# Kernel tuning notes

Hardware: AMD Instinct MI355X
Metric: run time of the kernel (lower is better)

## Reference

```python
import jax, jax.numpy as jnp
import numpy as np

F_DIM = 256
DFF = 2048      # torch TransformerEncoderLayer default dim_feedforward
NHEAD = 4
NCLS = 7
MAXLEN = 256
BATCH = 256
LN_EPS = 1e-5


def _layer_norm(x, g, b):
    m = x.mean(-1, keepdims=True)
    v = ((x - m) ** 2).mean(-1, keepdims=True)
    return (x - m) / jnp.sqrt(v + LN_EPS) * g + b


def _pos_encoding(n, d):
    # NOTE: original code builds PE over x.size(1) (the batch dim) -- kept faithfully.
    pos = jnp.arange(n, dtype=jnp.float32)[:, None]
    div = jnp.exp(jnp.arange(0, d, 2, dtype=jnp.float32) * (-np.log(10000.0) / d))
    pe = jnp.zeros((n, d), dtype=jnp.float32)
    pe = pe.at[:, 0::2].set(jnp.sin(pos * div))
    pe = pe.at[:, 1::2].set(jnp.cos(pos * div))
    return pe


def _mha(x, Wqkv, bqkv, Wo, bo):
    # x: [S, B, F]  (torch MHA default seq-first layout)
    S, B, F = x.shape
    hd = F // NHEAD
    qkv = x @ Wqkv.T + bqkv                      # [S, B, 3F]
    q, k, v = jnp.split(qkv, 3, axis=-1)
    rs = lambda t: t.reshape(S, B, NHEAD, hd).transpose(1, 2, 0, 3)  # [B, h, S, hd]
    q, k, v = rs(q), rs(k), rs(v)
    attn = jax.nn.softmax(jnp.einsum('bhsd,bhtd->bhst', q, k) / jnp.float32(np.sqrt(hd)), axis=-1)
    o = jnp.einsum('bhst,bhtd->bhsd', attn, v).transpose(2, 0, 1, 3).reshape(S, B, F)
    return o @ Wo.T + bo


def _forward(U_s, U_p, W_emb, b_emb, Wqkv, bqkv, Wo, bo, ln1_g, ln1_b,
             W1, b1, W2, b2, ln2_g, ln2_b, W_fc, b_fc, W_sm, b_sm, seq_lengths):
    L = np.asarray(seq_lengths)                   # static host lengths
    T, B, F = U_s.shape
    mask = jnp.arange(T)[:, None] < jnp.asarray(L)[None, :]        # [T, B] valid-turn mask
    bank_s = U_s * mask[:, :, None]               # zero-padded, as feature_transfer does
    # ---- ReasonMod / MultiTurnTransformer (post-LN encoder layer, eval mode) ----
    h = bank_s @ W_emb.T + b_emb
    h = h + _pos_encoding(B, F)                   # faithful quirk: PE over batch dim
    a_out = _mha(h, Wqkv, bqkv, Wo, bo)
    h1 = _layer_norm(h + a_out, ln1_g, ln1_b)
    ff = jax.nn.relu(h1 @ W1.T + b1) @ W2.T + b2
    h2 = _layer_norm(h1 + ff, ln2_g, ln2_b)
    q = h + h2                                    # [T, B, F]; identical for every t in the loop
    # ---- gather + segment-softmax + scatter-add attention pooling, all t at once ----
    e = jnp.einsum('ibf,tbf->tib', U_p, q)        # scores per (target t, turn i, conv b)
    e = jnp.where(mask[None, :, :], e, -1e30)
    a = jax.nn.softmax(e, axis=1) * mask[None, :, :]
    r = jnp.einsum('tib,ibf->tbf', a, U_p * mask[:, :, None])      # scatter_add equivalent
    rc = jnp.concatenate([bank_s, r], axis=-1)    # [T, B, 2F]
    hidden = jax.nn.relu(rc @ W_fc.T + b_fc)
    logp = jax.nn.log_softmax(hidden @ W_sm.T + b_sm, axis=2)      # [T, B, n_classes]
    rows = np.concatenate([np.arange(l) for l in L])
    cols = np.repeat(np.arange(B), L)
    return logp[rows, cols]                       # [total_tokens, n_classes]


def setup_inputs() -> dict:
    key = jax.random.key(0)
    ks = jax.random.split(key, 24)
    rn = lambda k, shape, s=0.05: jax.random.normal(k, shape, dtype=jnp.float32) * s
    F, D2 = F_DIM, 2 * F_DIM
    inp = {
        'U_s': jax.random.normal(ks[0], (MAXLEN, BATCH, F), dtype=jnp.float32),
        'U_p': jax.random.normal(ks[1], (MAXLEN, BATCH, F), dtype=jnp.float32),
        'W_emb': rn(ks[2], (F, F)), 'b_emb': jnp.zeros((F,), jnp.float32),
        'Wqkv': rn(ks[3], (3 * F, F)), 'bqkv': jnp.zeros((3 * F,), jnp.float32),
        'Wo': rn(ks[4], (F, F)), 'bo': jnp.zeros((F,), jnp.float32),
        'ln1_g': jnp.ones((F,), jnp.float32), 'ln1_b': jnp.zeros((F,), jnp.float32),
        'W1': rn(ks[5], (DFF, F)), 'b1': jnp.zeros((DFF,), jnp.float32),
        'W2': rn(ks[6], (F, DFF)), 'b2': jnp.zeros((F,), jnp.float32),
        'ln2_g': jnp.ones((F,), jnp.float32), 'ln2_b': jnp.zeros((F,), jnp.float32),
        'W_fc': rn(ks[7], (D2, D2)), 'b_fc': jnp.zeros((D2,), jnp.float32),
        'W_sm': rn(ks[8], (NCLS, D2)), 'b_sm': jnp.zeros((NCLS,), jnp.float32),
        'seq_lengths': jax.random.randint(ks[9], (BATCH,), MAXLEN // 2, MAXLEN + 1),
    }
    return inp


def reference(U_s, U_p, W_emb, b_emb, Wqkv, bqkv, Wo, bo, ln1_g, ln1_b,
              W1, b1, W2, b2, ln2_g, ln2_b, W_fc, b_fc, W_sm, b_sm, seq_lengths):
    return _forward(U_s, U_p, W_emb, b_emb, Wqkv, bqkv, Wo, bo, ln1_g, ln1_b,
                    W1, b1, W2, b2, ln2_g, ln2_b, W_fc, b_fc, W_sm, b_sm, seq_lengths)
```

## Files before the change

### kernel.cpp

```cpp
#include <hip/hip_runtime.h>

#define MTB 65536

typedef unsigned int uint;
typedef unsigned short ushort;

typedef _Float16 h8 __attribute__((ext_vector_type(8)));
typedef __attribute__((ext_vector_type(4))) float f4;

enum { E_BIAS=1, E_RELU=2, E_ACC=4, E_RES=8, E_PE=16, E_MASKA=32 };

__device__ __forceinline__ float ldsc(const float* p) { return *p; }
__device__ __forceinline__ float ldsc(const _Float16* p) { return (float)*p; }

__device__ __forceinline__ h8 uint4_to_h8(uint4 u) { return __builtin_bit_cast(h8, u); }

template<int EPI, int AMODE, int BMODE, typename CT, int CPL, typename RT, int RPL, int SWZ>
__global__ __launch_bounds__(256) void gemm_h(
    int M, int N, int K,
    const void* __restrict__ Ap, const void* __restrict__ Ap2, int lda, long batchA,
    const void* __restrict__ Bp, int ldw, long batchW,
    CT* __restrict__ C, long cplane, int ldc, long batchC,
    const float* __restrict__ bias,
    const RT* __restrict__ res, const RT* __restrict__ resLo,
    const float* __restrict__ pe,
    const int* __restrict__ seqlen)
{
    __shared__ _Float16 Ah[128][40];
    __shared__ _Float16 Al[(AMODE==3)?128:1][40];
    __shared__ _Float16 Bh[128][40];
    __shared__ _Float16 Bl[(BMODE==0)?128:1][40];

    const int z = blockIdx.z;
    C += (size_t)z * batchC;
    const float*    Af  = (const float*)Ap + (AMODE==0 ? (size_t)z*batchA : 0);
    const _Float16* Ahp = (const _Float16*)Ap + ((AMODE==2||AMODE==3) ? (size_t)z*batchA : 0);
    const _Float16* Alp = (const _Float16*)Ap2 + (AMODE==3 ? (size_t)z*batchA : 0);
    const float*    Bf  = (const float*)Bp + (BMODE!=2 ? (size_t)z*batchW : 0);
    const _Float16* Bhp = (const _Float16*)Bp;

    int bx = blockIdx.x, by = blockIdx.y;
    if (SWZ) {
        const int gx = gridDim.x;
        const int nwg = gx * gridDim.y;
        const int per = nwg >> 3;
        const int id = by * gx + bx;
        const int nid = (id & 7) * per + (id >> 3);
        bx = nid % gx; by = nid / gx;
    }
    const int m0 = by * 128, n0 = bx * 128;
    const int tid = threadIdx.x;
    const int lane = tid & 63, wid = tid >> 6;
    const int wr = wid >> 1, wc = wid & 1;

    f4 acc[4][4];
    {
        f4 zr = {0.f, 0.f, 0.f, 0.f};
        #pragma unroll
        for (int i = 0; i < 4; i++)
            #pragma unroll
            for (int j = 0; j < 4; j++) acc[i][j] = zr;
    }

    for (int k0 = 0; k0 < K; k0 += 32) {
        __syncthreads();
        if (AMODE == 0 || (AMODE == 4 && k0 < 256)) {
            #pragma unroll
            for (int i = 0; i < 4; i++) {
                const int row = i*32 + (tid>>3);
                const int cg  = (tid&7)<<2;
                const int m = m0 + row;
                float4 v; v.x=0.f; v.y=0.f; v.z=0.f; v.w=0.f;
                bool ok = true;
                if (EPI & E_MASKA) ok = ((m>>8) < seqlen[m&255]);
                if (ok) v = *(const float4*)(Af + (size_t)m*lda + k0 + cg);
                Ah[row][cg+0] = (_Float16)v.x;
                Ah[row][cg+1] = (_Float16)v.y;
                Ah[row][cg+2] = (_Float16)v.z;
                Ah[row][cg+3] = (_Float16)v.w;
            }
        } else if (AMODE == 4) {
            const _Float16* Ar = (const _Float16*)Ap2;
            const int row = tid >> 1;
            const int cg  = (tid & 1) << 4;
            const size_t off = (size_t)(m0 + row) * 256 + (k0 - 256) + cg;
            *(uint4*)&Ah[row][cg]     = *(const uint4*)(Ar + off);
            *(uint4*)&Ah[row][cg + 8] = *(const uint4*)(Ar + off + 8);
        } else {
            const int row = tid >> 1;
            const int cg  = (tid & 1) << 4;
            const size_t off = (size_t)(m0 + row) * lda + k0 + cg;
            *(uint4*)&Ah[row][cg]     = *(const uint4*)(Ahp + off);
            *(uint4*)&Ah[row][cg + 8] = *(const uint4*)(Ahp + off + 8);
            if (AMODE == 3) {
                *(uint4*)&Al[row][cg]     = *(const uint4*)(Alp + off);
                *(uint4*)&Al[row][cg + 8] = *(const uint4*)(Alp + off + 8);
            }
        }
        if (BMODE == 2) {
            const int row = tid >> 1;
            const int cg  = (tid & 1) << 4;
            const size_t off = (size_t)(n0 + row) * ldw + k0 + cg;
            *(uint4*)&Bh[row][cg]     = *(const uint4*)(Bhp + off);
            *(uint4*)&Bh[row][cg + 8] = *(const uint4*)(Bhp + off + 8);
        } else if (BMODE == 0) {
            #pragma unroll
            for (int i = 0; i < 4; i++) {
                const int row = i*32 + (tid>>3);
                const int cg  = (tid&7)<<2;
                float4 v = *(const float4*)(Bf + (size_t)(n0+row)*ldw + k0 + cg);
                _Float16 h0 = (_Float16)v.x, h1 = (_Float16)v.y,
                         h2 = (_Float16)v.z, h3 = (_Float16)v.w;
                Bh[row][cg+0]=h0; Bl[row][cg+0]=(_Float16)(v.x-(float)h0);
                Bh[row][cg+1]=h1; Bl[row][cg+1]=(_Float16)(v.y-(float)h1);
                Bh[row][cg+2]=h2; Bl[row][cg+2]=(_Float16)(v.z-(float)h2);
                Bh[row][cg+3]=h3; Bl[row][cg+3]=(_Float16)(v.w-(float)h3);
            }
        } else if (BMODE == 3) {
            #pragma unroll
            for (int i = 0; i < 4; i++) {
                const int row = i*32 + (tid>>3);
                const int cg  = (tid&7)<<2;
                float4 v = *(const float4*)(Bf + (size_t)(n0+row)*ldw + k0 + cg);
                Bh[row][cg+0]=(_Float16)v.x; Bh[row][cg+1]=(_Float16)v.y;
                Bh[row][cg+2]=(_Float16)v.z; Bh[row][cg+3]=(_Float16)v.w;
            }
        } else {
            #pragma unroll
            for (int i = 0; i < 4; i++) {
                const int kr = i*8 + (tid>>5);
                const int ng = (tid&31)<<2;
                float4 v = *(const float4*)(Bf + (size_t)(k0+kr)*ldw + n0 + ng);
                Bh[ng+0][kr] = (_Float16)v.x;
                Bh[ng+1][kr] = (_Float16)v.y;
                Bh[ng+2][kr] = (_Float16)v.z;
                Bh[ng+3][kr] = (_Float16)v.w;
            }
        }
        __syncthreads();
        const int lr = lane & 15, lk = (lane>>4)<<3;
        h8 ah[4], bh[4];
        #pragma unroll
        for (int i = 0; i < 4; i++) {
            ah[i] = *(const h8*)&Ah[wr*64 + i*16 + lr][lk];
            bh[i] = *(const h8*)&Bh[wc*64 + i*16 + lr][lk];
        }
        #pragma unroll
        for (int mi = 0; mi < 4; mi++)
            #pragma unroll
            for (int ni = 0; ni < 4; ni++)
                acc[mi][ni] = __builtin_amdgcn_mfma_f32_16x16x32_f16(ah[mi], bh[ni], acc[mi][ni], 0, 0, 0);
        if (AMODE == 3) {
            h8 al[4], bl[4];
            #pragma unroll
            for (int i = 0; i < 4; i++) {
                al[i] = *(const h8*)&Al[wr*64 + i*16 + lr][lk];
                bl[i] = *(const h8*)&Bl[wc*64 + i*16 + lr][lk];
            }
            #pragma unroll
            for (int mi = 0; mi < 4; mi++)
                #pragma unroll
                for (int ni = 0; ni < 4; ni++) {
                    acc[mi][ni] = __builtin_amdgcn_mfma_f32_16x16x32_f16(ah[mi], bl[ni], acc[mi][ni], 0, 0, 0);
                    acc[mi][ni] = __builtin_amdgcn_mfma_f32_16x16x32_f16(al[mi], bh[ni], acc[mi][ni], 0, 0, 0);
                }
        }
    }
    const int colb = n0 + wc*64;
    const int rowb = m0 + wr*64;
    #pragma unroll
    for (int ni = 0; ni < 4; ni++) {
        const int col = colb + ni*16 + (lane & 15);
        float bv = (EPI & E_BIAS) ? bias[col] : 0.f;
        #pragma unroll
        for (int mi = 0; mi < 4; mi++) {
            const int r0 = rowb + mi*16 + ((lane>>4)<<2);
            #pragma unroll
            for (int j = 0; j < 4; j++) {
                const int row = r0 + j;
                const size_t idx = (size_t)row*ldc + col;
                float v = acc[mi][ni][j] + bv;
                if (EPI & E_PE)  v += pe[((row & 255) << 8) + col];
                if (EPI & E_RES) {
                    v += ldsc(res + idx);
                    if (RPL) v += ldsc(resLo + idx);
                }
                CT* cp = C + idx;
                if (EPI & E_ACC) v += ldsc((const CT*)cp);
                if (EPI & E_RELU) v = fmaxf(v, 0.f);
                if (CPL) {
                    _Float16 hh = (_Float16)v;
                    *(_Float16*)cp = hh;
                    *((_Float16*)cp + cplane) = (_Float16)(v - (float)hh);
                } else if (sizeof(CT) == 2) {
                    *(_Float16*)cp = (_Float16)v;
                } else {
                    *(float*)cp = v;
                }
            }
        }
    }
}

__global__ __launch_bounds__(256) void ff_kernel(
    const _Float16* __restrict__ h1,
    const _Float16* __restrict__ W1p,
    const _Float16* __restrict__ W2p,
    const float* __restrict__ b1,
    const float* __restrict__ b2,
    float* __restrict__ res2)
{
    __shared__ _Float16 Bs[256][36];
    __shared__ _Float16 zt[64][136];
    const int m0 = blockIdx.x * 64;
    const int tid = threadIdx.x;
    const int lane = tid & 63, wid = tid >> 6;
    const int wr = wid >> 1, wc = wid & 1;
    const int lr = lane & 15, lg = lane >> 4;
    const int lk = lg << 3;
    const int l4 = lg << 2;
    const int srow = tid >> 1, sh = tid & 1;

    h8 af[2][8];
    #pragma unroll
    for (int mi = 0; mi < 2; mi++)
        #pragma unroll
        for (int ks = 0; ks < 8; ks++)
            af[mi][ks] = *(const h8*)(h1 + (size_t)(m0 + wr*32 + mi*16 + lr) * 256 + ks*32 + lk);

    f4 acc2[2][8];
    {
        f4 zr = {0.f,0.f,0.f,0.f};
        #pragma unroll
        for (int mi = 0; mi < 2; mi++)
            #pragma unroll
            for (int ni = 0; ni < 8; ni++) acc2[mi][ni] = zr;
    }

    uint4 p1a, p1b;
    uint4 p2[4];
    {
        const _Float16* g = W1p + (size_t)srow * 256 + sh*16;
        p1a = *(const uint4*)g; p1b = *(const uint4*)(g + 8);
    }

    for (int c = 0; c < 16; c++) {
        f4 acc1[2][4];
        {
            f4 zr = {0.f,0.f,0.f,0.f};
            #pragma unroll
            for (int mi = 0; mi < 2; mi++)
                #pragma unroll
                for (int ni = 0; ni < 4; ni++) acc1[mi][ni] = zr;
        }
        for (int ks = 0; ks < 8; ks++) {
            __syncthreads();
            {
                _Float16* d = &Bs[srow][sh*16];
                uint2 t0; t0.x=p1a.x; t0.y=p1a.y; *(uint2*)(d+0)  = t0;
                uint2 t1; t1.x=p1a.z; t1.y=p1a.w; *(uint2*)(d+4)  = t1;
                uint2 t2; t2.x=p1b.x; t2.y=p1b.y; *(uint2*)(d+8)  = t2;
                uint2 t3; t3.x=p1b.z; t3.y=p1b.w; *(uint2*)(d+12) = t3;
            }
            __syncthreads();
            if (ks < 7) {
                const _Float16* g = W1p + (size_t)(c*128 + srow) * 256 + (ks+1)*32 + sh*16;
                p1a = *(const uint4*)g; p1b = *(const uint4*)(g + 8);
            } else {
                const _Float16* g = W2p + (size_t)tid * 2048 + c*128;
                #pragma unroll
                for (int q = 0; q < 4; q++) p2[q] = *(const uint4*)(g + 8*q);
            }
            #pragma unroll
            for (int ni = 0; ni < 4; ni++) {
                const _Float16* s = &Bs[wc*64 + ni*16 + lr][lk];
                uint2 q0 = *(const uint2*)s;
                uint2 q1 = *(const uint2*)(s + 4);
                uint4 u; u.x=q0.x; u.y=q0.y; u.z=q1.x; u.w=q1.y;
                const h8 b = uint4_to_h8(u);
                acc1[0][ni] = __builtin_amdgcn_mfma_f32_16x16x32_f16(af[0][ks], b, acc1[0][ni], 0, 0, 0);
                acc1[1][ni] = __builtin_amdgcn_mfma_f32_16x16x32_f16(af[1][ks], b, acc1[1][ni], 0, 0, 0);
            }
        }
        #pragma unroll
        for (int ni = 0; ni < 4; ni++) {
            const float bv = b1[c*128 + wc*64 + ni*16 + lr];
            #pragma unroll
            for (int mi = 0; mi < 2; mi++)
                #pragma unroll
                for (int j = 0; j < 4; j++) {
                    float v = acc1[mi][ni][j] + bv;
                    v = fmaxf(v, 0.f);
                    zt[wr*32 + mi*16 + l4 + j][wc*64 + ni*16 + lr] = (_Float16)v;
                }
        }
        __syncthreads();
        for (int kk = 0; kk < 4; kk++) {
            if (kk) __syncthreads();
            {
                _Float16* d = &Bs[tid][0];
                #pragma unroll
                for (int q = 0; q < 4; q++) {
                    uint2 ta; ta.x=p2[q].x; ta.y=p2[q].y; *(uint2*)(d + 8*q)     = ta;
                    uint2 tb; tb.x=p2[q].z; tb.y=p2[q].w; *(uint2*)(d + 8*q + 4) = tb;
                }
            }
            __syncthreads();
            if (kk < 3) {
                const _Float16* g = W2p + (size_t)tid * 2048 + c*128 + (kk+1)*32;
                #pragma unroll
                for (int q = 0; q < 4; q++) p2[q] = *(const uint4*)(g + 8*q);
            } else if (c < 15) {
                const _Float16* g = W1p + (size_t)((c+1)*128 + srow) * 256 + sh*16;
                p1a = *(const uint4*)g; p1b = *(const uint4*)(g + 8);
            }
            const h8 a0 = *(const h8*)&zt[wr*32 +      lr][kk*32 + lk];
            const h8 a1 = *(const h8*)&zt[wr*32 + 16 + lr][kk*32 + lk];
            #pragma unroll
            for (int ni = 0; ni < 8; ni++) {
                const _Float16* s = &Bs[wc*128 + ni*16 + lr][lk];
                uint2 q0 = *(const uint2*)s;
                uint2 q1 = *(const uint2*)(s + 4);
                uint4 u; u.x=q0.x; u.y=q0.y; u.z=q1.x; u.w=q1.y;
                const h8 b = uint4_to_h8(u);
                acc2[0][ni] = __builtin_amdgcn_mfma_f32_16x16x32_f16(a0, b, acc2[0][ni], 0, 0, 0);
                acc2[1][ni] = __builtin_amdgcn_mfma_f32_16x16x32_f16(a1, b, acc2[1][ni], 0, 0, 0);
            }
        }
    }
    #pragma unroll
    for (int ni = 0; ni < 8; ni++) {
        const int col = wc*128 + ni*16 + lr;
        const float bv = b2[col];
        #pragma unroll
        for (int mi = 0; mi < 2; mi++) {
            const int rl = wr*32 + mi*16 + l4;
            #pragma unroll
            for (int j = 0; j < 4; j++) {
                const size_t idx = (size_t)(m0 + rl + j) * 256 + col;
                res2[idx] = acc2[mi][ni][j] + bv + (float)h1[idx];
            }
        }
    }
}

__global__ void cvt_kernel(const float* __restrict__ src, int ld, int cshift,
                           _Float16* __restrict__ dst, int total)
{
    const int i = blockIdx.x * 256 + threadIdx.x;
    if (i >= total) return;
    const int r = i >> cshift, c = i & ((1 << cshift) - 1);
    dst[i] = (_Float16)src[(size_t)r * ld + c];
}

__global__ __launch_bounds__(256) void attn_kernel(const _Float16* __restrict__ qkv,
                                                   _Float16* __restrict__ o)
{
    __shared__ _Float16 Kl[64][68];
    __shared__ _Float16 Vt[64][68];
    __shared__ _Float16 Pl[4][64][68];
    const int b = blockIdx.x, head = blockIdx.y;
    const _Float16* base = qkv + (size_t)b * 768 + head * 64;
    const int tid = threadIdx.x;
    const int lane = tid & 63, wid = tid >> 6;
    const int lr = lane & 15, lg = lane >> 4;
    const int lk = lg << 3;
    const int q0 = wid * 64;

    h8 qf[4][2];
    #pragma unroll
    for (int mi = 0; mi < 4; mi++)
        #pragma unroll
        for (int kk = 0; kk < 2; kk++)
            qf[mi][kk] = *(const h8*)(base + (size_t)(q0 + mi*16 + lr) * 196608 + kk*32 + lk);

    f4 oacc[4][4];
    float m_st[4][4], l_st[4][4];
    {
        f4 zr = {0.f,0.f,0.f,0.f};
        #pragma unroll
        for (int mi = 0; mi < 4; mi++)
            #pragma unroll
            for (int di = 0; di < 4; di++) oacc[mi][di] = zr;
        #pragma unroll
        for (int mi = 0; mi < 4; mi++)
            #pragma unroll
            for (int j = 0; j < 4; j++) { m_st[mi][j] = -1e30f; l_st[mi][j] = 0.f; }
    }

    for (int kt = 0; kt < 4; kt++) {
        __syncthreads();
        {
            const int row = tid >> 2, c0 = (tid & 3) << 4;
            const _Float16* rp = base + (size_t)(kt*64 + row) * 196608;
            *(uint4*)&Kl[row][c0]     = *(const uint4*)(rp + 256 + c0);
            *(uint4*)&Kl[row][c0 + 8] = *(const uint4*)(rp + 256 + c0 + 8);
            const h8 v0 = *(const h8*)(rp + 512 + c0);
            const h8 v1 = *(const h8*)(rp + 512 + c0 + 8);
            #pragma unroll
            for (int j = 0; j < 8; j++) {
                Vt[c0 + j][row]     = v0[j];
                Vt[c0 + 8 + j][row] = v1[j];
            }
        }
        __syncthreads();
        f4 sacc[4][4];
        {
            f4 zr = {0.f,0.f,0.f,0.f};
            #pragma unroll
            for (int mi = 0; mi < 4; mi++)
                #pragma unroll
                for (int ni = 0; ni < 4; ni++) sacc[mi][ni] = zr;
        }
        #pragma unroll
        for (int kk = 0; kk < 2; kk++) {
            h8 kf[4];
            #pragma unroll
            for (int ni = 0; ni < 4; ni++)
                kf[ni] = *(const h8*)&Kl[ni*16 + lr][kk*32 + lk];
            #pragma unroll
            for (int mi = 0; mi < 4; mi++)
                #pragma unroll
                for (int ni = 0; ni < 4; ni++)
                    sacc[mi][ni] = __builtin_amdgcn_mfma_f32_16x16x32_f16(qf[mi][kk], kf[ni], sacc[mi][ni], 0, 0, 0);
        }
        #pragma unroll
        for (int mi = 0; mi < 4; mi++)
            #pragma unroll
            for (int ni = 0; ni < 4; ni++)
                #pragma unroll
                for (int j = 0; j < 4; j++) sacc[mi][ni][j] *= 0.125f;
        #pragma unroll
        for (int mi = 0; mi < 4; mi++) {
            #pragma unroll
            for (int j = 0; j < 4; j++) {
                float tm = fmaxf(fmaxf(sacc[mi][0][j], sacc[mi][1][j]),
                                 fmaxf(sacc[mi][2][j], sacc[mi][3][j]));
                tm = fmaxf(tm, __shfl_xor(tm, 1));
                tm = fmaxf(tm, __shfl_xor(tm, 2));
                tm = fmaxf(tm, __shfl_xor(tm, 4));
                tm = fmaxf(tm, __shfl_xor(tm, 8));
                const float mn = fmaxf(m_st[mi][j], tm);
                const float sc = __expf(m_st[mi][j] - mn);
                m_st[mi][j] = mn;
                float ps = 0.f;
                #pragma unroll
                for (int ni = 0; ni < 4; ni++) {
                    const float p = __expf(sacc[mi][ni][j] - mn);
                    sacc[mi][ni][j] = p;
                    ps += p;
                }
                ps += __shfl_xor(ps, 1);
                ps += __shfl_xor(ps, 2);
                ps += __shfl_xor(ps, 4);
                ps += __shfl_xor(ps, 8);
                l_st[mi][j] = l_st[mi][j] * sc + ps;
                #pragma unroll
                for (int di = 0; di < 4; di++) oacc[mi][di][j] *= sc;
            }
        }
        #pragma unroll
        for (int mi = 0; mi < 4; mi++)
            #pragma unroll
            for (int ni = 0; ni < 4; ni++)
                #pragma unroll
                for (int j = 0; j < 4; j++)
                    Pl[wid][mi*16 + (lg<<2) + j][ni*16 + lr] = (_Float16)sacc[mi][ni][j];
        #pragma unroll
        for (int kk = 0; kk < 2; kk++) {
            h8 pf[4], vf[4];
            #pragma unroll
            for (int mi = 0; mi < 4; mi++)
                pf[mi] = *(const h8*)&Pl[wid][mi*16 + lr][kk*32 + lk];
            #pragma unroll
            for (int di = 0; di < 4; di++)
                vf[di] = *(const h8*)&Vt[di*16 + lr][kk*32 + lk];
            #pragma unroll
            for (int mi = 0; mi < 4; mi++)
                #pragma unroll
                for (int di = 0; di < 4; di++)
                    oacc[mi][di] = __builtin_amdgcn_mfma_f32_16x16x32_f16(pf[mi], vf[di], oacc[mi][di], 0, 0, 0);
        }
    }
    _Float16* obase = o + (size_t)b * 256 + head * 64;
    #pragma unroll
    for (int mi = 0; mi < 4; mi++) {
        #pragma unroll
        for (int j = 0; j < 4; j++) {
            const float inv = 1.f / l_st[mi][j];
            const size_t rowoff = (size_t)(q0 + mi*16 + (lg<<2) + j) * 65536;
            #pragma unroll
            for (int di = 0; di < 4; di++)
                obase[rowoff + di*16 + lr] = (_Float16)(oacc[mi][di][j] * inv);
        }
    }
}

template<int OPL, typename OT>
__global__ __launch_bounds__(256) void ln_kernel(const float* __restrict__ x,
    const float* __restrict__ g, const float* __restrict__ bt,
    const _Float16* __restrict__ addin, const _Float16* __restrict__ addinLo,
    OT* __restrict__ out, long oplane, int nrows)
{
    const int gid = blockIdx.x * 256 + threadIdx.x;
    const int row = gid >> 6;
    const int lane = threadIdx.x & 63;
    if (row >= nrows) return;
    const float* xr = x + (size_t)row * 256;
    float4 v = *(const float4*)(xr + (lane<<2));
    float s = v.x + v.y + v.z + v.w;
    #pragma unroll
    for (int off = 32; off > 0; off >>= 1) s += __shfl_xor(s, off, 64);
    const float mean = s * (1.0f/256.0f);
    const float dx = v.x-mean, dy = v.y-mean, dz = v.z-mean, dw = v.w-mean;
    float ss = dx*dx + dy*dy + dz*dz + dw*dw;
    #pragma unroll
    for (int off = 32; off > 0; off >>= 1) ss += __shfl_xor(ss, off, 64);
    const float inv = rsqrtf(ss * (1.0f/256.0f) + 1e-5f);
    const float4 gv = *(const float4*)(g + (lane<<2));
    const float4 bv = *(const float4*)(bt + (lane<<2));
    float ov[4];
    ov[0] = dx*inv*gv.x + bv.x;
    ov[1] = dy*inv*gv.y + bv.y;
    ov[2] = dz*inv*gv.z + bv.z;
    ov[3] = dw*inv*gv.w + bv.w;
    const size_t base = (size_t)row*256 + (lane<<2);
    if (addin) {
        #pragma unroll
        for (int j = 0; j < 4; j++) {
            ov[j] += (float)addin[base+j];
            if (addinLo) ov[j] += (float)addinLo[base+j];
        }
    }
    #pragma unroll
    for (int j = 0; j < 4; j++) {
        if (OPL) {
            _Float16 hh = (_Float16)ov[j];
            ((_Float16*)out)[base+j] = hh;
            ((_Float16*)out)[base+j+oplane] = (_Float16)(ov[j] - (float)hh);
        } else if (sizeof(OT) == 2) {
            ((_Float16*)out)[base+j] = (_Float16)ov[j];
        } else {
            ((float*)out)[base+j] = ov[j];
        }
    }
}

__global__ __launch_bounds__(256) void smax_kernel(float* __restrict__ e,
                                                   const int* __restrict__ seqlen)
{
    const int gid = blockIdx.x * 256 + threadIdx.x;
    const int row = gid >> 6;
    const int lane = threadIdx.x & 63;
    const int L = seqlen[row >> 8];
    float* er = e + (size_t)row * 256;
    float4 v = *(const float4*)(er + (lane<<2));
    const int i0 = lane << 2;
    const float x0 = (i0+0 < L) ? v.x : -1e30f;
    const float x1 = (i0+1 < L) ? v.y : -1e30f;
    const float x2 = (i0+2 < L) ? v.z : -1e30f;
    const float x3 = (i0+3 < L) ? v.w : -1e30f;
    float mx = fmaxf(fmaxf(x0,x1), fmaxf(x2,x3));
    #pragma unroll
    for (int off = 32; off > 0; off >>= 1) mx = fmaxf(mx, __shfl_xor(mx, off, 64));
    const float p0 = (i0+0 < L) ? __expf(x0-mx) : 0.f;
    const float p1 = (i0+1 < L) ? __expf(x1-mx) : 0.f;
    const float p2 = (i0+2 < L) ? __expf(x2-mx) : 0.f;
    const float p3 = (i0+3 < L) ? __expf(x3-mx) : 0.f;
    float s = p0+p1+p2+p3;
    #pragma unroll
    for (int off = 32; off > 0; off >>= 1) s += __shfl_xor(s, off, 64);
    const float inv = 1.f / s;
    v.x = p0*inv; v.y = p1*inv; v.z = p2*inv; v.w = p3*inv;
    *(float4*)(er + (lane<<2)) = v;
}

__global__ __launch_bounds__(256) void head_kernel(const _Float16* __restrict__ hidden,
    const float* __restrict__ Wsm, const float* __restrict__ bsm,
    const int* __restrict__ seqlen, const int* __restrict__ offs,
    float* __restrict__ out)
{
    const int gid = blockIdx.x * 256 + threadIdx.x;
    const int row = gid >> 6;
    const int lane = threadIdx.x & 63;
    if (row >= MTB) return;
    const int t = row >> 8, b = row & 255;
    if (t >= seqlen[b]) return;
    const _Float16* hr = hidden + (size_t)row * 512;
    const h8 hu = *(const h8*)(hr + lane*8);
    float hv[8];
    #pragma unroll
    for (int j = 0; j < 8; j++) hv[j] = (float)hu[j];
    float lg[7];
    #pragma unroll
    for (int c = 0; c < 7; c++) {
        const float* wr = Wsm + c*512 + lane*8;
        const float4 w0 = *(const float4*)wr;
        const float4 w1 = *(const float4*)(wr + 4);
        float acc = hv[0]*w0.x + hv[1]*w0.y + hv[2]*w0.z + hv[3]*w0.w
                  + hv[4]*w1.x + hv[5]*w1.y + hv[6]*w1.z + hv[7]*w1.w;
        #pragma unroll
        for (int off = 32; off > 0; off >>= 1) acc += __shfl_xor(acc, off, 64);
        lg[c] = acc + bsm[c];
    }
    float mx = lg[0];
    #pragma unroll
    for (int c = 1; c < 7; c++) mx = fmaxf(mx, lg[c]);
    float s = 0.f;
    #pragma unroll
    for (int c = 0; c < 7; c++) s += __expf(lg[c] - mx);
    const float lse = mx + logf(s);
    if (lane == 0) {
        float* orow = out + (size_t)(offs[b] + t) * 7;
        #pragma unroll
        for (int c = 0; c < 7; c++) orow[c] = lg[c] - lse;
    }
}

__global__ void pe_kernel(float* __restrict__ pe)
{
    const int idx = blockIdx.x * 256 + threadIdx.x;
    const int b = idx >> 8, f = idx & 255;
    const int j = f >> 1;
    const float div = expf(-9.210340371976184f * (2.0f * j) * (1.0f/256.0f));
    const float arg = (float)b * div;
    pe[idx] = (f & 1) ? cosf(arg) : sinf(arg);
}

__global__ void prefix_kernel(const int* __restrict__ L, int* __restrict__ offs)
{
    if (threadIdx.x == 0) {
        int acc = 0;
        for (int i = 0; i < 256; i++) { offs[i] = acc; acc += L[i]; }
        offs[256] = acc;
    }
}

__global__ void sentinel_kernel(float* __restrict__ out, float v)
{
    if (threadIdx.x == 0) out[0] = v;
}

extern "C" void kernel_launch(void* const* d_in, const int* in_sizes, int n_in,
                              void* d_out, int out_size, void* d_ws, size_t ws_size,
                              hipStream_t stream)
{
    const float* U_s   = (const float*)d_in[0];
    const float* U_p   = (const float*)d_in[1];
    const float* W_emb = (const float*)d_in[2];
    const float* b_emb = (const float*)d_in[3];
    const float* Wqkv  = (const float*)d_in[4];
    const float* bqkv  = (const float*)d_in[5];
    const float* Wo    = (const float*)d_in[6];
    const float* bo    = (const float*)d_in[7];
    const float* ln1_g = (const float*)d_in[8];
    const float* ln1_b = (const float*)d_in[9];
    const float* W1    = (const float*)d_in[10];
    const float* b1    = (const float*)d_in[11];
    const float* W2    = (const float*)d_in[12];
    const float* b2    = (const float*)d_in[13];
    const float* ln2_g = (const float*)d_in[14];
    const float* ln2_b = (const float*)d_in[15];
    const float* W_fc  = (const float*)d_in[16];
    const float* b_fc  = (const float*)d_in[17];
    const float* W_sm  = (const float*)d_in[18];
    const float* b_sm  = (const float*)d_in[19];
    const int*   seqlen= (const int*)d_in[20];
    float* out = (float*)d_out;

    const size_t MiB = 1024*1024;
    const size_t KiB = 1024;
    char* ws = (char*)d_ws;
    if (ws_size < 193*MiB) {
        sentinel_kernel<<<dim3(1), dim3(64), 0, stream>>>(out, -(float)(ws_size / MiB));
        return;
    }
    const long PL = 16*1024*1024;
    _Float16* h_hi = (_Float16*)(ws);
    _Float16* h_lo = (_Float16*)(ws + 32*MiB);
    int*      offs = (int*)(ws + 64*MiB);
    char*     slot = ws + 64*MiB + 8*KiB;
    _Float16* qkv  = (_Float16*)(ws + 65*MiB);
    _Float16* o    = (_Float16*)(ws + 161*MiB);
    float*    res1 = (float*)(ws + 65*MiB);
    float*    res2 = res1;
    _Float16* h1   = (_Float16*)(ws + 161*MiB);
    _Float16* w1p  = (_Float16*)(ws + 129*MiB);
    _Float16* w2p  = (_Float16*)(ws + 130*MiB);
    _Float16* q_hi = (_Float16*)(ws + 129*MiB);
    float*    e    = (float*)(ws + 65*MiB);
    _Float16* r    = (_Float16*)(ws);
    _Float16* hid  = (_Float16*)(ws + 129*MiB);

    prefix_kernel<<<dim3(1), dim3(64), 0, stream>>>(seqlen, offs);

    _Float16* wp  = (_Float16*)slot;
    float*    pe  = (float*)(slot + 512*KiB);

    cvt_kernel<<<dim3(256), 256, 0, stream>>>(W_emb, 256, 8, wp, 65536);
    pe_kernel<<<dim3(256), dim3(256), 0, stream>>>(pe);
    gemm_h<E_BIAS|E_PE|E_MASKA, 0, 2, _Float16, 1, float, 0, 1>
        <<<dim3(2,512,1), 256, 0, stream>>>(
        MTB,256,256, U_s,nullptr,256,0, wp,256,0, h_hi,PL,256,0,
        b_emb, (const float*)nullptr, nullptr, pe, seqlen);

    cvt_kernel<<<dim3(768), 256, 0, stream>>>(Wqkv, 256, 8, wp, 196608);
    gemm_h<E_BIAS, 2, 2, _Float16, 0, float, 0, 1>
        <<<dim3(6,512,1), 256, 0, stream>>>(
        MTB,768,256, h_hi,nullptr,256,0, wp,256,0, qkv,0,768,0,
        bqkv, (const float*)nullptr, nullptr, nullptr, nullptr);

    attn_kernel<<<dim3(256,4), 256, 0, stream>>>(qkv, o);

    cvt_kernel<<<dim3(256), 256, 0, stream>>>(Wo, 256, 8, wp, 65536);
    gemm_h<E_BIAS|E_RES, 2, 2, float, 0, _Float16, 1, 1>
        <<<dim3(2,512,1), 256, 0, stream>>>(
        MTB,256,256, o,nullptr,256,0, wp,256,0, res1,0,256,0,
        bo, h_hi, h_lo, nullptr, nullptr);

    ln_kernel<0, _Float16><<<dim3(MTB/4), 256, 0, stream>>>(
        res1, ln1_g, ln1_b, nullptr, nullptr, h1, 0, MTB);

    cvt_kernel<<<dim3(2048), 256, 0, stream>>>(W1, 256, 8, w1p, 524288);
    cvt_kernel<<<dim3(2048), 256, 0, stream>>>(W2, 2048, 11, w2p, 524288);
    ff_kernel<<<dim3(1024), 256, 0, stream>>>(h1, w1p, w2p, b1, b2, res2);

    ln_kernel<0, _Float16><<<dim3(MTB/4), 256, 0, stream>>>(
        res2, ln2_g, ln2_b, h_hi, h_lo, q_hi, 0, MTB);

    gemm_h<0, 2, 3, float, 0, float, 0, 0>
        <<<dim3(2,2,256), 256, 0, stream>>>(
        256,256,256, q_hi,nullptr,65536,256, U_p,65536,256, e,0,256,65536,
        nullptr, (const float*)nullptr, nullptr, nullptr, nullptr);

    smax_kernel<<<dim3(MTB/4), 256, 0, stream>>>(e, seqlen);

    gemm_h<0, 0, 1, _Float16, 0, float, 0, 0>
        <<<dim3(2,2,256), 256, 0, stream>>>(
        256,256,256, e,nullptr,256,65536, U_p,65536,256, r,0,65536,256,
        nullptr, (const float*)nullptr, nullptr, nullptr, nullptr);

    cvt_kernel<<<dim3(1024), 256, 0, stream>>>(W_fc, 512, 9, wp, 262144);
    gemm_h<E_BIAS|E_RELU|E_MASKA, 4, 2, _Float16, 0, float, 0, 1>
        <<<dim3(4,512,1), 256, 0, stream>>>(
        MTB,512,512, U_s,r,256,0, wp,512,0, hid,0,512,0,
        b_fc, (const float*)nullptr, nullptr, nullptr, seqlen);

    head_kernel<<<dim3(MTB/4), 256, 0, stream>>>(hid, W_sm, b_sm, seqlen, offs, out);
}
```

Before: 902.4 us.

## Double-buffer LDS weight tiles in fused FFN kernel to halve barriers

Makes the shared-memory weight tile in ff_kernel double-buffered for both the W1 and W2 GEMM phases. Each step now writes the next tile into the alternate buffer after issuing its MFMAs, so one barrier per k-step replaces two. Global prefetches move one step further ahead. The aim is to cut barrier stalls and let LDS stores overlap with MFMA work, at the cost of doubling the Bs footprint, which may lower occupancy.

```diff
diff --git a/kernel.cpp b/kernel.cpp
--- a/kernel.cpp
+++ b/kernel.cpp
@@ -210,7 +210,7 @@
     const float* __restrict__ b2,
     float* __restrict__ res2)
 {
-    __shared__ _Float16 Bs[256][36];
+    __shared__ _Float16 Bs[2][256][36];
     __shared__ _Float16 zt[64][136];
     const int m0 = blockIdx.x * 64;
     const int tid = threadIdx.x;
@@ -253,27 +253,23 @@
                 #pragma unroll
                 for (int ni = 0; ni < 4; ni++) acc1[mi][ni] = zr;
         }
+        {
+            _Float16* d = &Bs[0][srow][sh*16];
+            uint2 t0; t0.x=p1a.x; t0.y=p1a.y; *(uint2*)(d+0)  = t0;
+            uint2 t1; t1.x=p1a.z; t1.y=p1a.w; *(uint2*)(d+4)  = t1;
+            uint2 t2; t2.x=p1b.x; t2.y=p1b.y; *(uint2*)(d+8)  = t2;
+            uint2 t3; t3.x=p1b.z; t3.y=p1b.w; *(uint2*)(d+12) = t3;
+        }
+        {
+            const _Float16* g = W1p + (size_t)(c*128 + srow) * 256 + 32 + sh*16;
+            p1a = *(const uint4*)g; p1b = *(const uint4*)(g + 8);
+        }
+        __syncthreads();
         for (int ks = 0; ks < 8; ks++) {
-            __syncthreads();
-            {
-                _Float16* d = &Bs[srow][sh*16];
-                uint2 t0; t0.x=p1a.x; t0.y=p1a.y; *(uint2*)(d+0)  = t0;
-                uint2 t1; t1.x=p1a.z; t1.y=p1a.w; *(uint2*)(d+4)  = t1;
-                uint2 t2; t2.x=p1b.x; t2.y=p1b.y; *(uint2*)(d+8)  = t2;
-                uint2 t3; t3.x=p1b.z; t3.y=p1b.w; *(uint2*)(d+12) = t3;
-            }
-            __syncthreads();
-            if (ks < 7) {
-                const _Float16* g = W1p + (size_t)(c*128 + srow) * 256 + (ks+1)*32 + sh*16;
-                p1a = *(const uint4*)g; p1b = *(const uint4*)(g + 8);
-            } else {
-                const _Float16* g = W2p + (size_t)tid * 2048 + c*128;
-                #pragma unroll
-                for (int q = 0; q < 4; q++) p2[q] = *(const uint4*)(g + 8*q);
-            }
+            const int cur = ks & 1;
             #pragma unroll
             for (int ni = 0; ni < 4; ni++) {
-                const _Float16* s = &Bs[wc*64 + ni*16 + lr][lk];
+                const _Float16* s = &Bs[cur][wc*64 + ni*16 + lr][lk];
                 uint2 q0 = *(const uint2*)s;
                 uint2 q1 = *(const uint2*)(s + 4);
                 uint4 u; u.x=q0.x; u.y=q0.y; u.z=q1.x; u.w=q1.y;
@@ -281,6 +277,24 @@
                 acc1[0][ni] = __builtin_amdgcn_mfma_f32_16x16x32_f16(af[0][ks], b, acc1[0][ni], 0, 0, 0);
                 acc1[1][ni] = __builtin_amdgcn_mfma_f32_16x16x32_f16(af[1][ks], b, acc1[1][ni], 0, 0, 0);
             }
+            if (ks < 7) {
+                {
+                    _Float16* d = &Bs[cur^1][srow][sh*16];
+                    uint2 t0; t0.x=p1a.x; t0.y=p1a.y; *(uint2*)(d+0)  = t0;
+                    uint2 t1; t1.x=p1a.z; t1.y=p1a.w; *(uint2*)(d+4)  = t1;
+                    uint2 t2; t2.x=p1b.x; t2.y=p1b.y; *(uint2*)(d+8)  = t2;
+                    uint2 t3; t3.x=p1b.z; t3.y=p1b.w; *(uint2*)(d+12) = t3;
+                }
+                if (ks < 6) {
+                    const _Float16* g = W1p + (size_t)(c*128 + srow) * 256 + (ks+2)*32 + sh*16;
+                    p1a = *(const uint4*)g; p1b = *(const uint4*)(g + 8);
+                } else {
+                    const _Float16* g = W2p + (size_t)tid * 2048 + c*128;
+                    #pragma unroll
+                    for (int q = 0; q < 4; q++) p2[q] = *(const uint4*)(g + 8*q);
+                }
+                __syncthreads();
+            }
         }
         #pragma unroll
         for (int ni = 0; ni < 4; ni++) {
@@ -294,37 +308,52 @@
                     zt[wr*32 + mi*16 + l4 + j][wc*64 + ni*16 + lr] = (_Float16)v;
                 }
         }
+        {
+            _Float16* d = &Bs[0][tid][0];
+            #pragma unroll
+            for (int q = 0; q < 4; q++) {
+                uint2 ta; ta.x=p2[q].x; ta.y=p2[q].y; *(uint2*)(d + 8*q)     = ta;
+                uint2 tb; tb.x=p2[q].z; tb.y=p2[q].w; *(uint2*)(d + 8*q + 4) = tb;
+            }
+        }
+        {
+            const _Float16* g = W2p + (size_t)tid * 2048 + c*128 + 32;
+            #pragma unroll
+            for (int q = 0; q < 4; q++) p2[q] = *(const uint4*)(g + 8*q);
+        }
         __syncthreads();
         for (int kk = 0; kk < 4; kk++) {
-            if (kk) __syncthreads();
-            {
-                _Float16* d = &Bs[tid][0];
-                #pragma unroll
-                for (int q = 0; q < 4; q++) {
-                    uint2 ta; ta.x=p2[q].x; ta.y=p2[q].y; *(uint2*)(d + 8*q)     = ta;
-                    uint2 tb; tb.x=p2[q].z; tb.y=p2[q].w; *(uint2*)(d + 8*q + 4) = tb;
-                }
-            }
-            __syncthreads();
-            if (kk < 3) {
-                const _Float16* g = W2p + (size_t)tid * 2048 + c*128 + (kk+1)*32;
-                #pragma unroll
-                for (int q = 0; q < 4; q++) p2[q] = *(const uint4*)(g + 8*q);
-            } else if (c < 15) {
-                const _Float16* g = W1p + (size_t)((c+1)*128 + srow) * 256 + sh*16;
-                p1a = *(const uint4*)g; p1b = *(const uint4*)(g + 8);
-            }
+            const int cur = kk & 1;
             const h8 a0 = *(const h8*)&zt[wr*32 +      lr][kk*32 + lk];
             const h8 a1 = *(const h8*)&zt[wr*32 + 16 + lr][kk*32 + lk];
             #pragma unroll
             for (int ni = 0; ni < 8; ni++) {
-                const _Float16* s = &Bs[wc*128 + ni*16 + lr][lk];
+                const _Float16* s = &Bs[cur][wc*128 + ni*16 + lr][lk];
                 uint2 q0 = *(const uint2*)s;
                 uint2 q1 = *(const uint2*)(s + 4);
                 uint4 u; u.x=q0.x; u.y=q0.y; u.z=q1.x; u.w=q1.y;
                 const h8 b = uint4_to_h8(u);
                 acc2[0][ni] = __builtin_amdgcn_mfma_f32_16x16x32_f16(a0, b, acc2[0][ni], 0, 0, 0);
                 acc2[1][ni] = __builtin_amdgcn_mfma_f32_16x16x32_f16(a1, b, acc2[1][ni], 0, 0, 0);
+            }
+            if (kk < 3) {
+                {
+                    _Float16* d = &Bs[cur^1][tid][0];
+                    #pragma unroll
+                    for (int q = 0; q < 4; q++) {
+                        uint2 ta; ta.x=p2[q].x; ta.y=p2[q].y; *(uint2*)(d + 8*q)     = ta;
+                        uint2 tb; tb.x=p2[q].z; tb.y=p2[q].w; *(uint2*)(d + 8*q + 4) = tb;
+                    }
+                }
+                if (kk < 2) {
+                    const _Float16* g = W2p + (size_t)tid * 2048 + c*128 + (kk+2)*32;
+                    #pragma unroll
+                    for (int q = 0; q < 4; q++) p2[q] = *(const uint4*)(g + 8*q);
+                } else if (c < 15) {
+                    const _Float16* g = W1p + (size_t)((c+1)*128 + srow) * 256 + sh*16;
+                    p1a = *(const uint4*)g; p1b = *(const uint4*)(g + 8);
+                }
+                __syncthreads();
             }
         }
     }
```

New measurement: 935.4 us. +3.6%, slower.
